# Performance work log

Measured on AMD Instinct MI355X. Metric: run time of the kernel, lower is better.

## Reference

```python
import jax, jax.numpy as jnp
import numpy as np

N_QUBITS = 4
N_LAYERS = 2
DIM = 2 ** N_QUBITS


def _cnot_perm(c, t, n=N_QUBITS):
    # statevector index bit for wire w is at shift (n-1-w)
    idx = np.arange(2 ** n)
    cbit = (idx >> (n - 1 - c)) & 1
    return np.where(cbit == 1, idx ^ (1 << (n - 1 - t)), idx)


def _apply_cnot(state, c, t):
    # state: [B, 2,2,2,2]; CNOT is a basis permutation (its own inverse)
    B = state.shape[0]
    flat = state.reshape(B, DIM)
    return flat[:, _cnot_perm(c, t)].reshape(state.shape)


def _apply_1q(state, U, wire):
    # shared 2x2 gate U on given wire
    st = jnp.moveaxis(state, wire + 1, -1)
    st = jnp.einsum('b...a,ca->b...c', st, U)
    return jnp.moveaxis(st, -1, wire + 1)


def _quantum_circuit(z, weights):
    """AngleEmbedding(RY) + StronglyEntanglingLayers, PauliZ expvals.
    z: [B, n_qubits] angles, weights: [L, n_qubits, 3]. Returns [B, n_qubits]."""
    n = N_QUBITS
    B = z.shape[0]
    state = jnp.zeros((B, DIM), jnp.complex64).at[:, 0].set(1.0)
    state = state.reshape((B,) + (2,) * n)
    # Angle embedding: batched RY(z_w) on each wire
    for w in range(n):
        a = z[:, w] * 0.5
        c, s = jnp.cos(a), jnp.sin(a)
        U = jnp.stack([jnp.stack([c, -s], -1), jnp.stack([s, c], -1)], -2)  # [B,2,2]
        st = jnp.moveaxis(state, w + 1, -1)
        st = jnp.einsum('b...a,bca->b...c', st, U.astype(jnp.complex64))
        state = jnp.moveaxis(st, -1, w + 1)
    # StronglyEntanglingLayers
    for l in range(N_LAYERS):
        for w in range(n):
            phi, theta, omega = weights[l, w, 0], weights[l, w, 1], weights[l, w, 2]
            ct, st_ = jnp.cos(theta * 0.5), jnp.sin(theta * 0.5)
            e_m = jnp.exp(-0.5j * (phi + omega).astype(jnp.complex64))
            e_d = jnp.exp(0.5j * (phi - omega).astype(jnp.complex64))
            U = jnp.stack([
                jnp.stack([e_m * ct, -e_d * st_]),
                jnp.stack([jnp.conj(e_d) * st_, jnp.conj(e_m) * ct]),
            ])  # Rot(phi,theta,omega) = RZ(omega) RY(theta) RZ(phi)
            state = _apply_1q(state, U, w)
        r = (l % (n - 1)) + 1
        for w in range(n):
            state = _apply_cnot(state, w, (w + r) % n)
    probs = state.real ** 2 + state.imag ** 2  # [B,2,2,2,2]
    evs = []
    rest = tuple(range(1, n))
    for w in range(n):
        p = jnp.moveaxis(probs, w + 1, 1)
        evs.append(jnp.sum(p[:, 0], axis=rest) - jnp.sum(p[:, 1], axis=rest))
    return jnp.stack(evs, -1)


def setup_inputs() -> dict:
    key = jax.random.key(0)
    ks = jax.random.split(key, 6)
    B, C, H, W = 16, 256, 128, 128
    return {
        'x': jax.random.normal(ks[0], (B, C, H, W), jnp.float32),
        'enc_w': jax.random.normal(ks[1], (N_QUBITS, C), jnp.float32) / np.sqrt(C),
        'enc_b': jax.random.normal(ks[2], (N_QUBITS,), jnp.float32) * 0.01,
        'qweights': jax.random.uniform(ks[3], (N_LAYERS, N_QUBITS, 3), jnp.float32, 0.0, 2.0 * np.pi),
        'proj_w': jax.random.normal(ks[4], (C, N_QUBITS), jnp.float32) / np.sqrt(N_QUBITS),
        'proj_b': jax.random.normal(ks[5], (C,), jnp.float32) * 0.01,
    }


def reference(x, enc_w, enc_b, qweights, proj_w, proj_b):
    pooled = jnp.mean(x, axis=(2, 3))                      # AdaptiveAvgPool2d(1)+Flatten -> [B,C]
    z = jnp.tanh(pooled @ enc_w.T + enc_b)                 # [B, n_qubits]
    refined = _quantum_circuit(z, qweights)                # [B, n_qubits]
    gates = jax.nn.sigmoid(refined @ proj_w.T + proj_b)    # [B, C]
    return x + x * gates[:, :, None, None]
```

## Files before the change

kernel.cpp:

```cpp
#include <hip/hip_runtime.h>
#include <math.h>

#define NQ 4
#define NL 2
#define DIM 16
#define BATCH 16
#define CH 256
#define HW 16384

typedef float floatx4 __attribute__((ext_vector_type(4)));

__global__ void pool_kernel(const float* __restrict__ x, float* __restrict__ pooled) {
    const int bc = blockIdx.x;
    const floatx4* x4 = (const floatx4*)(x + (size_t)bc * HW);
    const int tid = threadIdx.x;
    float s = 0.f;
#pragma unroll
    for (int k = 0; k < 16; ++k) {
        floatx4 v = x4[tid + k * 256];
        s += v.x + v.y + v.z + v.w;
    }
#pragma unroll
    for (int off = 32; off > 0; off >>= 1) s += __shfl_down(s, off, 64);
    __shared__ float partial[4];
    if ((tid & 63) == 0) partial[tid >> 6] = s;
    __syncthreads();
    if (tid == 0)
        pooled[bc] = (partial[0] + partial[1] + partial[2] + partial[3]) * (1.0f / HW);
}

__global__ void gate_kernel(const float* __restrict__ pooled,
                            const float* __restrict__ enc_w,
                            const float* __restrict__ enc_b,
                            const float* __restrict__ qw,
                            const float* __restrict__ proj_w,
                            const float* __restrict__ proj_b,
                            float* __restrict__ gates1p) {
    __shared__ float sp[BATCH * CH];
    __shared__ float sz[BATCH][NQ];
    __shared__ float sref[BATCH][NQ];
    const int tid = threadIdx.x;

    for (int i = tid; i < BATCH * CH; i += 256) sp[i] = pooled[i];
    __syncthreads();

    if (tid < BATCH * NQ) {
        const int b = tid >> 2, q = tid & 3;
        float acc = enc_b[q];
        for (int c = 0; c < CH; ++c) acc += sp[b * CH + c] * enc_w[q * CH + c];
        sz[b][q] = tanhf(acc);
    }
    __syncthreads();

    if (tid < BATCH) {
        const int b = tid;
        float re[DIM], im[DIM];
#pragma unroll
        for (int i = 0; i < DIM; ++i) { re[i] = 0.f; im[i] = 0.f; }
        re[0] = 1.f;

        for (int w = 0; w < NQ; ++w) {
            const float a = sz[b][w] * 0.5f;
            const float cc = cosf(a), ss = sinf(a);
            const int m = 1 << (3 - w);
#pragma unroll
            for (int i = 0; i < DIM; ++i) {
                if (i & m) continue;
                const int j = i | m;
                const float r0 = cc * re[i] - ss * re[j];
                const float i0 = cc * im[i] - ss * im[j];
                const float r1 = ss * re[i] + cc * re[j];
                const float i1 = ss * im[i] + cc * im[j];
                re[i] = r0; im[i] = i0; re[j] = r1; im[j] = i1;
            }
        }

        for (int l = 0; l < NL; ++l) {
            for (int w = 0; w < NQ; ++w) {
                const float phi = qw[(l * NQ + w) * 3 + 0];
                const float th  = qw[(l * NQ + w) * 3 + 1];
                const float om  = qw[(l * NQ + w) * 3 + 2];
                const float ct = cosf(0.5f * th), st = sinf(0.5f * th);
                const float am = -0.5f * (phi + om);
                const float ad =  0.5f * (phi - om);
                const float emr = cosf(am), emi = sinf(am);
                const float edr = cosf(ad), edi = sinf(ad);
                const float u00r =  emr * ct, u00i =  emi * ct;
                const float u01r = -edr * st, u01i = -edi * st;
                const float u10r =  edr * st, u10i = -edi * st;
                const float u11r =  emr * ct, u11i = -emi * ct;
                const int m = 1 << (3 - w);
#pragma unroll
                for (int i = 0; i < DIM; ++i) {
                    if (i & m) continue;
                    const int j = i | m;
                    const float ar = re[i], ai = im[i], br = re[j], bi = im[j];
                    re[i] = u00r * ar - u00i * ai + u01r * br - u01i * bi;
                    im[i] = u00r * ai + u00i * ar + u01r * bi + u01i * br;
                    re[j] = u10r * ar - u10i * ai + u11r * br - u11i * bi;
                    im[j] = u10r * ai + u10i * ar + u11r * bi + u11i * br;
                }
            }
            const int r = (l % (NQ - 1)) + 1;
            for (int w = 0; w < NQ; ++w) {
                const int t = (w + r) % NQ;
                const int cm = 1 << (3 - w);
                const int tm = 1 << (3 - t);
#pragma unroll
                for (int i = 0; i < DIM; ++i) {
                    if ((i & cm) && !(i & tm)) {
                        const int j = i | tm;
                        float tr = re[i]; re[i] = re[j]; re[j] = tr;
                        float ti = im[i]; im[i] = im[j]; im[j] = ti;
                    }
                }
            }
        }

        float p[DIM];
#pragma unroll
        for (int i = 0; i < DIM; ++i) p[i] = re[i] * re[i] + im[i] * im[i];
        for (int w = 0; w < NQ; ++w) {
            const int m = 1 << (3 - w);
            float ev = 0.f;
#pragma unroll
            for (int i = 0; i < DIM; ++i) ev += (i & m) ? -p[i] : p[i];
            sref[b][w] = ev;
        }
    }
    __syncthreads();

    const int c = tid;
    const float pw0 = proj_w[c * NQ + 0], pw1 = proj_w[c * NQ + 1];
    const float pw2 = proj_w[c * NQ + 2], pw3 = proj_w[c * NQ + 3];
    const float pb = proj_b[c];
    for (int b = 0; b < BATCH; ++b) {
        const float acc = sref[b][0] * pw0 + sref[b][1] * pw1 +
                          sref[b][2] * pw2 + sref[b][3] * pw3 + pb;
        gates1p[b * CH + c] = 1.f + 1.f / (1.f + expf(-acc));
    }
}

__global__ void scale_kernel(const float* __restrict__ x,
                             const float* __restrict__ gates1p,
                             float* __restrict__ out) {
    const floatx4* x4 = (const floatx4*)x;
    floatx4* o4 = (floatx4*)out;
    const int base = blockIdx.x * 2048 + threadIdx.x;
    const float g = gates1p[blockIdx.x >> 1];
    floatx4 v[8];
#pragma unroll
    for (int k = 0; k < 8; ++k) v[k] = x4[base + k * 256];
#pragma unroll
    for (int k = 0; k < 8; ++k) {
        v[k] *= g;
        __builtin_nontemporal_store(v[k], &o4[base + k * 256]);
    }
}

extern "C" void kernel_launch(void* const* d_in, const int* in_sizes, int n_in,
                              void* d_out, int out_size, void* d_ws, size_t ws_size,
                              hipStream_t stream) {
    const float* x      = (const float*)d_in[0];
    const float* enc_w  = (const float*)d_in[1];
    const float* enc_b  = (const float*)d_in[2];
    const float* qw     = (const float*)d_in[3];
    const float* proj_w = (const float*)d_in[4];
    const float* proj_b = (const float*)d_in[5];
    float* out = (float*)d_out;

    float* pooled  = (float*)d_ws;
    float* gates1p = pooled + BATCH * CH;

    pool_kernel<<<BATCH * CH, 256, 0, stream>>>(x, pooled);
    gate_kernel<<<1, 256, 0, stream>>>(pooled, enc_w, enc_b, qw, proj_w, proj_b, gates1p);
    scale_kernel<<<8192, 256, 0, stream>>>(x, gates1p, out);
}
```

Measured before the change: 149.9 us.

## Fuse gate computation into scale kernel, recomputing per-block quantum circuit

Merges the single-block gate kernel with the scale kernel. Each of the 1024 blocks now computes its batch's encoder projection, runs the 4-qubit circuit on one thread and derives gates for its 4 channel slices, then scales those slices. This removes one launch and the serialized single-block gate stage, at the cost of redundant circuit computation per block and a serial thread-0 phase before streaming. The pool kernel also switches to nontemporal loads.

```diff
diff --git a/kernel.cpp b/kernel.cpp
--- a/kernel.cpp
+++ b/kernel.cpp
@@ -7,6 +7,8 @@
 #define BATCH 16
 #define CH 256
 #define HW 16384
+#define SPB 4
+#define NBLK (BATCH * CH / SPB)
 
 typedef float floatx4 __attribute__((ext_vector_type(4)));
 
@@ -17,7 +19,7 @@
     float s = 0.f;
 #pragma unroll
     for (int k = 0; k < 16; ++k) {
-        floatx4 v = x4[tid + k * 256];
+        floatx4 v = __builtin_nontemporal_load(&x4[tid + k * 256]);
         s += v.x + v.y + v.z + v.w;
     }
 #pragma unroll
@@ -29,38 +31,47 @@
         pooled[bc] = (partial[0] + partial[1] + partial[2] + partial[3]) * (1.0f / HW);
 }
 
-__global__ void gate_kernel(const float* __restrict__ pooled,
-                            const float* __restrict__ enc_w,
-                            const float* __restrict__ enc_b,
-                            const float* __restrict__ qw,
-                            const float* __restrict__ proj_w,
-                            const float* __restrict__ proj_b,
-                            float* __restrict__ gates1p) {
-    __shared__ float sp[BATCH * CH];
-    __shared__ float sz[BATCH][NQ];
-    __shared__ float sref[BATCH][NQ];
+__global__ void fused_gate_scale(
+    const float* __restrict__ x,
+    const float* __restrict__ enc_w,
+    const float* __restrict__ enc_b,
+    const float* __restrict__ qw,
+    const float* __restrict__ proj_w,
+    const float* __restrict__ proj_b,
+    const float* __restrict__ pooled,
+    float* __restrict__ out)
+{
     const int tid = threadIdx.x;
+    const int slice0 = blockIdx.x * SPB;
+    const int b = slice0 >> 8;
 
-    for (int i = tid; i < BATCH * CH; i += 256) sp[i] = pooled[i];
-    __syncthreads();
+    __shared__ float sz[NQ];
+    __shared__ float sevs[NQ];
+    __shared__ float sgate[SPB];
 
-    if (tid < BATCH * NQ) {
-        const int b = tid >> 2, q = tid & 3;
-        float acc = enc_b[q];
-        for (int c = 0; c < CH; ++c) acc += sp[b * CH + c] * enc_w[q * CH + c];
-        sz[b][q] = tanhf(acc);
+    {
+        const int wid = tid >> 6, lane = tid & 63;
+        const float* prow = pooled + b * CH;
+        float acc = 0.f;
+#pragma unroll
+        for (int j = 0; j < 4; ++j) {
+            const int c = lane * 4 + j;
+            acc += prow[c] * enc_w[wid * CH + c];
+        }
+#pragma unroll
+        for (int off = 32; off > 0; off >>= 1) acc += __shfl_down(acc, off, 64);
+        if (lane == 0) sz[wid] = tanhf(acc + enc_b[wid]);
     }
     __syncthreads();
 
-    if (tid < BATCH) {
-        const int b = tid;
+    if (tid == 0) {
         float re[DIM], im[DIM];
 #pragma unroll
         for (int i = 0; i < DIM; ++i) { re[i] = 0.f; im[i] = 0.f; }
         re[0] = 1.f;
 
         for (int w = 0; w < NQ; ++w) {
-            const float a = sz[b][w] * 0.5f;
+            const float a = sz[w] * 0.5f;
             const float cc = cosf(a), ss = sinf(a);
             const int m = 1 << (3 - w);
 #pragma unroll
@@ -125,36 +136,32 @@
             float ev = 0.f;
 #pragma unroll
             for (int i = 0; i < DIM; ++i) ev += (i & m) ? -p[i] : p[i];
-            sref[b][w] = ev;
+            sevs[w] = ev;
         }
     }
     __syncthreads();
 
-    const int c = tid;
-    const float pw0 = proj_w[c * NQ + 0], pw1 = proj_w[c * NQ + 1];
-    const float pw2 = proj_w[c * NQ + 2], pw3 = proj_w[c * NQ + 3];
-    const float pb = proj_b[c];
-    for (int b = 0; b < BATCH; ++b) {
-        const float acc = sref[b][0] * pw0 + sref[b][1] * pw1 +
-                          sref[b][2] * pw2 + sref[b][3] * pw3 + pb;
-        gates1p[b * CH + c] = 1.f + 1.f / (1.f + expf(-acc));
+    if (tid < SPB) {
+        const int c = (slice0 & 255) + tid;
+        const float acc = sevs[0] * proj_w[c * NQ + 0] + sevs[1] * proj_w[c * NQ + 1] +
+                          sevs[2] * proj_w[c * NQ + 2] + sevs[3] * proj_w[c * NQ + 3] +
+                          proj_b[c];
+        sgate[tid] = 1.f + 1.f / (1.f + expf(-acc));
     }
-}
+    __syncthreads();
 
-__global__ void scale_kernel(const float* __restrict__ x,
-                             const float* __restrict__ gates1p,
-                             float* __restrict__ out) {
-    const floatx4* x4 = (const floatx4*)x;
-    floatx4* o4 = (floatx4*)out;
-    const int base = blockIdx.x * 2048 + threadIdx.x;
-    const float g = gates1p[blockIdx.x >> 1];
-    floatx4 v[8];
+    for (int s = 0; s < SPB; ++s) {
+        const float gt = sgate[s];
+        const floatx4* x4 = (const floatx4*)(x + (size_t)(slice0 + s) * HW);
+        floatx4* o4 = (floatx4*)(out + (size_t)(slice0 + s) * HW);
+        floatx4 v[16];
 #pragma unroll
-    for (int k = 0; k < 8; ++k) v[k] = x4[base + k * 256];
+        for (int k = 0; k < 16; ++k) v[k] = __builtin_nontemporal_load(&x4[tid + k * 256]);
 #pragma unroll
-    for (int k = 0; k < 8; ++k) {
-        v[k] *= g;
-        __builtin_nontemporal_store(v[k], &o4[base + k * 256]);
+        for (int k = 0; k < 16; ++k) {
+            v[k] *= gt;
+            __builtin_nontemporal_store(v[k], &o4[tid + k * 256]);
+        }
     }
 }
 
@@ -168,11 +175,9 @@
     const float* proj_w = (const float*)d_in[4];
     const float* proj_b = (const float*)d_in[5];
     float* out = (float*)d_out;
-
-    float* pooled  = (float*)d_ws;
-    float* gates1p = pooled + BATCH * CH;
+    float* pooled = (float*)d_ws;
 
     pool_kernel<<<BATCH * CH, 256, 0, stream>>>(x, pooled);
-    gate_kernel<<<1, 256, 0, stream>>>(pooled, enc_w, enc_b, qw, proj_w, proj_b, gates1p);
-    scale_kernel<<<8192, 256, 0, stream>>>(x, gates1p, out);
+    fused_gate_scale<<<NBLK, 256, 0, stream>>>(x, enc_w, enc_b, qw,
+                                               proj_w, proj_b, pooled, out);
 }
```

After: 173.8 us. 15.9% more time.
